# Kernel optimization log

Measured on AMD Instinct MI355X. Metric: run time of the kernel, lower is better.

Reference implementation:

```python
import jax, jax.numpy as jnp
import numpy as np

TOP_K = 8
N_EXPERTS = 64
ALPHA = 0.001
EPS = 1e-9


def setup_inputs() -> dict:
    key = jax.random.key(0)
    k1, k2 = jax.random.split(key)
    B, S, H, E = 4, 4096, 2048, N_EXPERTS
    hidden_states = jax.random.normal(k1, (B, S, H), dtype=jnp.float32)
    # kaiming_uniform_(a=sqrt(5)) on [E,H] -> bound = 1/sqrt(H)
    bound = 1.0 / np.sqrt(H)
    weight = jax.random.uniform(k2, (E, H), dtype=jnp.float32, minval=-bound, maxval=bound)
    return {"hidden_states": hidden_states, "weight": weight}


def reference(hidden_states, weight):
    B, S, H = hidden_states.shape
    E = weight.shape[0]
    x = hidden_states.reshape(-1, H)                     # [N, H], N = B*S
    logits = jnp.einsum('nh,eh->ne', x, weight)          # [N, E]
    scores = jax.nn.sigmoid(logits)                      # sigmoid affinity (DeepSeek-V3 style)

    topk_weight, topk_idx = jax.lax.top_k(scores, TOP_K)  # [N, K]
    # norm_topk_prob = True and top_k > 1
    denom = topk_weight.sum(axis=-1, keepdims=True) + EPS
    topk_weight = topk_weight / denom

    # aux load-balance loss (training, alpha > 0); scatter-count instead of one_hot
    N = x.shape[0]
    counts = jnp.zeros((E,), dtype=jnp.float32).at[topk_idx.reshape(-1)].add(1.0)
    load = counts / (N * TOP_K)                          # == one_hot.mean(dim=(0,1))
    prob_raw = scores / (scores.sum(axis=-1, keepdims=True) + EPS)
    prob = prob_raw.mean(axis=0)
    prob = prob / (prob.sum() + EPS)
    aux_loss = ALPHA * (load * prob).sum() * E

    return topk_idx, topk_weight, aux_loss
```

## Files before the change

kernel.cpp:

```cpp
#include <hip/hip_runtime.h>
#include <math.h>

#define N_TOK 16384
#define HDIM  2048
#define NEXP  64
#define TOPK  8
#define NKS   4
#define KSEG  (HDIM / NKS)

#define PART_OFF  0
#define WT_OFF    (32u << 20)
#define STATS_OFF (33u << 20)

typedef double d4 __attribute__((ext_vector_type(4)));

__global__ __launch_bounds__(256) void conv_wt_kernel(const float* __restrict__ W,
                                                      double* __restrict__ Wt) {
    int i = blockIdx.x * 256 + threadIdx.x;
    int k = i >> 6, e = i & 63;
    Wt[i] = (double)W[(size_t)e * HDIM + k];
}

__global__ void mfma_probe_kernel(int* __restrict__ flag) {
    const int l = threadIdx.x;
    const int i16 = l & 15, q = l >> 4;
    const int r4 = l >> 2,  m4 = l & 3;
    int fv = 0;
#pragma unroll
    for (int ai = 0; ai < 2; ++ai)
#pragma unroll
    for (int bi = 0; bi < 2; ++bi) {
        const int ra = ai ? r4 : i16, ka = ai ? m4 : q;
        const int cb = bi ? r4 : i16, kb = bi ? m4 : q;
        double a = (double)(ra * 4 + ka + 1);
        double b = (double)((kb + 1) * 100 + 3 * cb);
        d4 acc = {0., 0., 0., 0.};
        acc = __builtin_amdgcn_mfma_f64_16x16x4f64(a, b, acc, 0, 0, 0);
#pragma unroll
        for (int sf = 0; sf < 2; ++sf)
#pragma unroll
        for (int tr = 0; tr < 2; ++tr) {
            int ok = 1;
#pragma unroll
            for (int r = 0; r < 4; ++r) {
                const int p   = sf ? (q + 4 * r) : (4 * q + r);
                const int row = tr ? i16 : p;
                const int col = tr ? p : i16;
                double ref = 0.0;
#pragma unroll
                for (int k = 0; k < 4; ++k)
                    ref += (double)(row * 4 + k + 1) * (double)((k + 1) * 100 + 3 * col);
                ok &= (acc[r] == ref);
            }
            if (__all(ok) && fv == 0) fv = 1 + ai * 8 + bi * 4 + sf * 2 + tr;
        }
    }
    if (l == 0) *flag = fv;
}

__global__ __launch_bounds__(256) void gemm_mfma_kernel(const float* __restrict__ X,
                                                        const double* __restrict__ Wt,
                                                        const int* __restrict__ flag,
                                                        double* __restrict__ part) {
    const int f = *flag;
    if (f == 0) return;
    const int fb = f - 1;
    const int ai = (fb >> 3) & 1, bi = (fb >> 2) & 1;
    const int sf = (fb >> 1) & 1, tr = fb & 1;

    const int tt  = blockIdx.x >> 2;
    const int ks  = blockIdx.x & 3;
    const int tid = threadIdx.x;
    const int l   = tid & 63;
    const int wv  = tid >> 6;
    const int wr  = wv >> 1, wc = wv & 1;
    const int tok0 = tt * 64;
    const int k0   = ks * KSEG;

    const int i16 = l & 15, q = l >> 4, r4 = l >> 2, m4 = l & 3;
    const int ra = ai ? r4 : i16, ka = ai ? m4 : q;
    const int cb = bi ? r4 : i16, kb = bi ? m4 : q;

    __shared__ double xs[64][34];
    __shared__ double wsh[32][66];

    d4 acc[2][2];
#pragma unroll
    for (int i = 0; i < 2; ++i)
#pragma unroll
        for (int j = 0; j < 2; ++j) acc[i][j] = (d4){0., 0., 0., 0.};

    const int xr = tid >> 2;
    const int xc = (tid & 3) * 8;
    const float* xg = X + (size_t)(tok0 + xr) * HDIM + k0 + xc;
    const int wk = tid >> 3;
    const int we = (tid & 7) * 8;
    const double* wg = Wt + (size_t)(k0 + wk) * NEXP + we;

    float4  px0 = *(const float4*)xg;
    float4  px1 = *(const float4*)(xg + 4);
    double2 pw0 = *(const double2*)(wg);
    double2 pw1 = *(const double2*)(wg + 2);
    double2 pw2 = *(const double2*)(wg + 4);
    double2 pw3 = *(const double2*)(wg + 6);

    const double* pa0 = &xs[wr * 32 + ra][ka];
    const double* pa1 = &xs[wr * 32 + 16 + ra][ka];
    const double* pb0 = &wsh[kb][wc * 32 + cb];
    const double* pb1 = &wsh[kb][wc * 32 + 16 + cb];

    for (int c = 0; c < KSEG / 32; ++c) {
        __syncthreads();
        {
            double2 t;
            t.x = (double)px0.x; t.y = (double)px0.y; *(double2*)&xs[xr][xc]     = t;
            t.x = (double)px0.z; t.y = (double)px0.w; *(double2*)&xs[xr][xc + 2] = t;
            t.x = (double)px1.x; t.y = (double)px1.y; *(double2*)&xs[xr][xc + 4] = t;
            t.x = (double)px1.z; t.y = (double)px1.w; *(double2*)&xs[xr][xc + 6] = t;
            *(double2*)&wsh[wk][we]     = pw0;
            *(double2*)&wsh[wk][we + 2] = pw1;
            *(double2*)&wsh[wk][we + 4] = pw2;
            *(double2*)&wsh[wk][we + 6] = pw3;
        }
        __syncthreads();
        if (c + 1 < KSEG / 32) {
            const float*  xn = xg + (c + 1) * 32;
            const double* wn = wg + (size_t)(c + 1) * 32 * NEXP;
            px0 = *(const float4*)xn;
            px1 = *(const float4*)(xn + 4);
            pw0 = *(const double2*)(wn);
            pw1 = *(const double2*)(wn + 2);
            pw2 = *(const double2*)(wn + 4);
            pw3 = *(const double2*)(wn + 6);
        }
#pragma unroll
        for (int kq = 0; kq < 8; ++kq) {
            double a0 = pa0[kq * 4];
            double a1 = pa1[kq * 4];
            double b0 = pb0[(size_t)kq * 4 * 66];
            double b1 = pb1[(size_t)kq * 4 * 66];
            acc[0][0] = __builtin_amdgcn_mfma_f64_16x16x4f64(a0, b0, acc[0][0], 0, 0, 0);
            acc[0][1] = __builtin_amdgcn_mfma_f64_16x16x4f64(a0, b1, acc[0][1], 0, 0, 0);
            acc[1][0] = __builtin_amdgcn_mfma_f64_16x16x4f64(a1, b0, acc[1][0], 0, 0, 0);
            acc[1][1] = __builtin_amdgcn_mfma_f64_16x16x4f64(a1, b1, acc[1][1], 0, 0, 0);
        }
    }

    double* pbase = part + (size_t)ks * N_TOK * NEXP;
#pragma unroll
    for (int rt = 0; rt < 2; ++rt)
#pragma unroll
        for (int ct = 0; ct < 2; ++ct)
#pragma unroll
            for (int r = 0; r < 4; ++r) {
                const int p    = sf ? (q + 4 * r) : (4 * q + r);
                const int dtok = tr ? i16 : p;
                const int dex  = tr ? p : i16;
                const int tok  = tok0 + wr * 32 + rt * 16 + dtok;
                const int ex   = wc * 32 + ct * 16 + dex;
                pbase[(size_t)tok * NEXP + ex] = acc[rt][ct][r];
            }
}

__global__ __launch_bounds__(512, 4) void gemm_valu_kernel(const float* __restrict__ X,
                                                           const double* __restrict__ Wt,
                                                           const int* __restrict__ flag,
                                                           double* __restrict__ part) {
    if (*flag != 0) return;
    const int tt   = blockIdx.x >> 2;
    const int ks   = blockIdx.x & 3;
    const int tid  = threadIdx.x;
    const int lane = tid & 63;
    const int wv   = tid >> 6;
    const int tok0 = tt * 64;
    const int k0   = ks * KSEG;

    __shared__ double xs[64][18];
    __shared__ double wsh[16][66];

    double acc[8];
#pragma unroll
    for (int t = 0; t < 8; ++t) acc[t] = 0.0;

    const int sx_tok = tid >> 3;
    const int sx_k   = (tid & 7) * 2;
    const float* xg  = X + (size_t)(tok0 + sx_tok) * HDIM + k0 + sx_k;
    const int sw_k = tid >> 5;
    const int sw_e = (tid & 31) * 2;
    const double* wg = Wt + (size_t)(k0 + sw_k) * NEXP + sw_e;

    float2  px = *(const float2*)xg;
    double2 pw = *(const double2*)wg;

    for (int c = 0; c < KSEG / 16; ++c) {
        __syncthreads();
        {
            double2 xv; xv.x = (double)px.x; xv.y = (double)px.y;
            *(double2*)&xs[sx_tok][sx_k] = xv;
            *(double2*)&wsh[sw_k][sw_e]  = pw;
        }
        __syncthreads();
        if (c + 1 < KSEG / 16) {
            px = *(const float2*)(xg + (c + 1) * 16);
            pw = *(const double2*)(wg + (size_t)(c + 1) * 16 * NEXP);
        }
        double wr_[16];
#pragma unroll
        for (int j = 0; j < 16; ++j) wr_[j] = wsh[j][lane];
#pragma unroll
        for (int t = 0; t < 8; ++t) {
            const int tr = wv * 8 + t;
#pragma unroll
            for (int kp = 0; kp < 8; ++kp) {
                double2 xv = *(const double2*)&xs[tr][kp * 2];
                acc[t] = fma(xv.x, wr_[kp * 2],     acc[t]);
                acc[t] = fma(xv.y, wr_[kp * 2 + 1], acc[t]);
            }
        }
    }

    double* pb = part + ((size_t)ks * N_TOK + tok0 + wv * 8) * NEXP + lane;
#pragma unroll
    for (int t = 0; t < 8; ++t)
        pb[(size_t)t * NEXP] = acc[t];
}

__global__ __launch_bounds__(256) void topk_kernel(const double* __restrict__ part,
                                                   float* __restrict__ outIdx,
                                                   float* __restrict__ outW,
                                                   float* __restrict__ stats) {
    __shared__ float sc_s[32][65];
    __shared__ float lds_counts[NEXP];
    __shared__ float psum_part[4][NEXP];
    const int tid  = threadIdx.x;
    const int lane = tid & 63;
    const int w    = tid >> 6;
    if (tid < NEXP) lds_counts[tid] = 0.f;

    const int t0 = blockIdx.x * 32;
#pragma unroll
    for (int p = 0; p < 8; ++p) {
        const int idx = p * 256 + tid;
        const int t   = idx >> 6;
        const int e   = idx & 63;
        const double* pp = part + ((size_t)(t0 + t)) * NEXP + e;
        double l = (pp[0] + pp[(size_t)N_TOK * NEXP]) +
                   (pp[2 * (size_t)N_TOK * NEXP] + pp[3 * (size_t)N_TOK * NEXP]);
        sc_s[t][e] = (float)(1.0 / (1.0 + exp(-l)));
    }
    __syncthreads();

    float ps = 0.f;
    for (int i = 0; i < 8; ++i) {
        const int tloc = w * 8 + i;
        const int t    = t0 + tloc;
        float s = sc_s[tloc][lane];

        float rs = s;
#pragma unroll
        for (int off = 32; off; off >>= 1) rs += __shfl_xor(rs, off);
        ps += s / (rs + 1e-9f);

        float cur = s;
        float denom = 0.f;
        int   wi = 0;
        float wv = 0.f;
#pragma unroll
        for (int k = 0; k < TOPK; ++k) {
            float m = cur; int mi = lane;
#pragma unroll
            for (int off = 32; off; off >>= 1) {
                float om = __shfl_xor(m, off);
                int   oi = __shfl_xor(mi, off);
                if (om > m || (om == m && oi < mi)) { m = om; mi = oi; }
            }
            denom += m;
            if (lane == k)  { wi = mi; wv = m; }
            if (lane == mi) cur = -1e30f;
        }
        if (lane < TOPK) {
            outIdx[(size_t)t * TOPK + lane] = (float)wi;
            outW  [(size_t)t * TOPK + lane] = wv / (denom + 1e-9f);
            atomicAdd(&lds_counts[wi], 1.f);
        }
    }
    psum_part[w][lane] = ps;
    __syncthreads();
    if (tid < NEXP) {
        float tot = psum_part[0][tid] + psum_part[1][tid] +
                    psum_part[2][tid] + psum_part[3][tid];
        atomicAdd(&stats[tid], tot);
        atomicAdd(&stats[NEXP + tid], lds_counts[tid]);
    }
}

__global__ void aux_kernel(const float* __restrict__ stats, float* __restrict__ out) {
    const int e = threadIdx.x;
    float prob = stats[e] / (float)N_TOK;
    float cnt  = stats[NEXP + e];
    float loadf = cnt / ((float)N_TOK * TOPK);
    float S = prob;
#pragma unroll
    for (int off = 32; off; off >>= 1) S += __shfl_xor(S, off);
    float pn = prob / (S + 1e-9f);
    float v  = loadf * pn;
#pragma unroll
    for (int off = 32; off; off >>= 1) v += __shfl_xor(v, off);
    if (e == 0) out[2 * N_TOK * TOPK] = 0.001f * v * (float)NEXP;
}

extern "C" void kernel_launch(void* const* d_in, const int* in_sizes, int n_in,
                              void* d_out, int out_size, void* d_ws, size_t ws_size,
                              hipStream_t stream) {
    (void)in_sizes; (void)n_in; (void)out_size; (void)ws_size;
    const float* X = (const float*)d_in[0];
    const float* W = (const float*)d_in[1];
    float* out = (float*)d_out;
    char*  ws  = (char*)d_ws;
    double* part  = (double*)(ws + PART_OFF);
    double* Wt    = (double*)(ws + WT_OFF);
    float*  stats = (float*)(ws + STATS_OFF);
    int*    flag  = (int*)(stats + 128);

    hipMemsetAsync(stats, 0, 132 * sizeof(float), stream);
    conv_wt_kernel<<<512, 256, 0, stream>>>(W, Wt);
    mfma_probe_kernel<<<1, 64, 0, stream>>>(flag);
    gemm_mfma_kernel<<<1024, 256, 0, stream>>>(X, Wt, flag, part);
    gemm_valu_kernel<<<1024, 512, 0, stream>>>(X, Wt, flag, part);
    topk_kernel<<<512, 256, 0, stream>>>(part, out, out + N_TOK * TOPK, stats);
    aux_kernel<<<1, 64, 0, stream>>>(stats, out);
}
```

Measured before the change: 148.5 us.

## Drop weight transpose kernel; read fp32 weights directly with k-permuted shared layout

Removes the separate kernel that converted the weight matrix to a transposed fp64 copy. Both GEMM kernels now load the fp32 weights directly from their original [E,H] layout and convert to double while staging into shared memory. The MFMA kernel stores X and W tiles with the same k-major-per-row layout, using a permuted k ordering so each lane can fetch two operands per double2 LDS read. This saves one kernel launch and a workspace round trip, but the global weight loads become scalar strided reads.

New measurement: 154.0 us. 3.7% more time.

```diff
diff --git a/kernel.cpp b/kernel.cpp
--- a/kernel.cpp
+++ b/kernel.cpp
@@ -7,19 +7,13 @@
 #define TOPK  8
 #define NKS   4
 #define KSEG  (HDIM / NKS)
+#define KCH   32
+#define NCH   (KSEG / KCH)
 
 #define PART_OFF  0
-#define WT_OFF    (32u << 20)
 #define STATS_OFF (33u << 20)
 
 typedef double d4 __attribute__((ext_vector_type(4)));
-
-__global__ __launch_bounds__(256) void conv_wt_kernel(const float* __restrict__ W,
-                                                      double* __restrict__ Wt) {
-    int i = blockIdx.x * 256 + threadIdx.x;
-    int k = i >> 6, e = i & 63;
-    Wt[i] = (double)W[(size_t)e * HDIM + k];
-}
 
 __global__ void mfma_probe_kernel(int* __restrict__ flag) {
     const int l = threadIdx.x;
@@ -59,7 +53,7 @@
 }
 
 __global__ __launch_bounds__(256) void gemm_mfma_kernel(const float* __restrict__ X,
-                                                        const double* __restrict__ Wt,
+                                                        const float* __restrict__ W,
                                                         const int* __restrict__ flag,
                                                         double* __restrict__ part) {
     const int f = *flag;
@@ -81,8 +75,8 @@
     const int ra = ai ? r4 : i16, ka = ai ? m4 : q;
     const int cb = bi ? r4 : i16, kb = bi ? m4 : q;
 
-    __shared__ double xs[64][34];
-    __shared__ double wsh[32][66];
+    __shared__ double Xs[64][34];
+    __shared__ double Ws[64][34];
 
     d4 acc[2][2];
 #pragma unroll
@@ -90,59 +84,58 @@
 #pragma unroll
         for (int j = 0; j < 2; ++j) acc[i][j] = (d4){0., 0., 0., 0.};
 
-    const int xr = tid >> 2;
-    const int xc = (tid & 3) * 8;
-    const float* xg = X + (size_t)(tok0 + xr) * HDIM + k0 + xc;
-    const int wk = tid >> 3;
-    const int we = (tid & 7) * 8;
-    const double* wg = Wt + (size_t)(k0 + wk) * NEXP + we;
-
-    float4  px0 = *(const float4*)xg;
-    float4  px1 = *(const float4*)(xg + 4);
-    double2 pw0 = *(const double2*)(wg);
-    double2 pw1 = *(const double2*)(wg + 2);
-    double2 pw2 = *(const double2*)(wg + 4);
-    double2 pw3 = *(const double2*)(wg + 6);
-
-    const double* pa0 = &xs[wr * 32 + ra][ka];
-    const double* pa1 = &xs[wr * 32 + 16 + ra][ka];
-    const double* pb0 = &wsh[kb][wc * 32 + cb];
-    const double* pb1 = &wsh[kb][wc * 32 + 16 + cb];
-
-    for (int c = 0; c < KSEG / 32; ++c) {
+    const int rs = tid >> 2, cu = tid & 3;
+    const float* xg = X + (size_t)(tok0 + rs) * HDIM + k0 + cu;
+    const float* wg = W + (size_t)rs * HDIM + k0 + cu;
+
+    float fx[8], fw[8];
+#pragma unroll
+    for (int j = 0; j < 4; ++j) {
+        fx[2 * j]     = xg[8 * j];
+        fx[2 * j + 1] = xg[8 * j + 4];
+        fw[2 * j]     = wg[8 * j];
+        fw[2 * j + 1] = wg[8 * j + 4];
+    }
+
+    for (int c = 0; c < NCH; ++c) {
         __syncthreads();
-        {
-            double2 t;
-            t.x = (double)px0.x; t.y = (double)px0.y; *(double2*)&xs[xr][xc]     = t;
-            t.x = (double)px0.z; t.y = (double)px0.w; *(double2*)&xs[xr][xc + 2] = t;
-            t.x = (double)px1.x; t.y = (double)px1.y; *(double2*)&xs[xr][xc + 4] = t;
-            t.x = (double)px1.z; t.y = (double)px1.w; *(double2*)&xs[xr][xc + 6] = t;
-            *(double2*)&wsh[wk][we]     = pw0;
-            *(double2*)&wsh[wk][we + 2] = pw1;
-            *(double2*)&wsh[wk][we + 4] = pw2;
-            *(double2*)&wsh[wk][we + 6] = pw3;
+#pragma unroll
+        for (int j = 0; j < 4; ++j) {
+            double2 dx; dx.x = (double)fx[2 * j]; dx.y = (double)fx[2 * j + 1];
+            double2 dw; dw.x = (double)fw[2 * j]; dw.y = (double)fw[2 * j + 1];
+            *(double2*)&Xs[rs][8 * cu + 2 * j] = dx;
+            *(double2*)&Ws[rs][8 * cu + 2 * j] = dw;
         }
         __syncthreads();
-        if (c + 1 < KSEG / 32) {
-            const float*  xn = xg + (c + 1) * 32;
-            const double* wn = wg + (size_t)(c + 1) * 32 * NEXP;
-            px0 = *(const float4*)xn;
-            px1 = *(const float4*)(xn + 4);
-            pw0 = *(const double2*)(wn);
-            pw1 = *(const double2*)(wn + 2);
-            pw2 = *(const double2*)(wn + 4);
-            pw3 = *(const double2*)(wn + 6);
-        }
-#pragma unroll
-        for (int kq = 0; kq < 8; ++kq) {
-            double a0 = pa0[kq * 4];
-            double a1 = pa1[kq * 4];
-            double b0 = pb0[(size_t)kq * 4 * 66];
-            double b1 = pb1[(size_t)kq * 4 * 66];
-            acc[0][0] = __builtin_amdgcn_mfma_f64_16x16x4f64(a0, b0, acc[0][0], 0, 0, 0);
-            acc[0][1] = __builtin_amdgcn_mfma_f64_16x16x4f64(a0, b1, acc[0][1], 0, 0, 0);
-            acc[1][0] = __builtin_amdgcn_mfma_f64_16x16x4f64(a1, b0, acc[1][0], 0, 0, 0);
-            acc[1][1] = __builtin_amdgcn_mfma_f64_16x16x4f64(a1, b1, acc[1][1], 0, 0, 0);
+        if (c + 1 < NCH) {
+            const float* xn = xg + (c + 1) * KCH;
+            const float* wn = wg + (c + 1) * KCH;
+#pragma unroll
+            for (int j = 0; j < 4; ++j) {
+                fx[2 * j]     = xn[8 * j];
+                fx[2 * j + 1] = xn[8 * j + 4];
+                fw[2 * j]     = wn[8 * j];
+                fw[2 * j + 1] = wn[8 * j + 4];
+            }
+        }
+        const double* pa0 = &Xs[wr * 32 + ra][8 * ka];
+        const double* pa1 = &Xs[wr * 32 + 16 + ra][8 * ka];
+        const double* pb0 = &Ws[wc * 32 + cb][8 * kb];
+        const double* pb1 = &Ws[wc * 32 + 16 + cb][8 * kb];
+#pragma unroll
+        for (int t = 0; t < 4; ++t) {
+            double2 a0 = *(const double2*)(pa0 + 2 * t);
+            double2 a1 = *(const double2*)(pa1 + 2 * t);
+            double2 b0 = *(const double2*)(pb0 + 2 * t);
+            double2 b1 = *(const double2*)(pb1 + 2 * t);
+            acc[0][0] = __builtin_amdgcn_mfma_f64_16x16x4f64(a0.x, b0.x, acc[0][0], 0, 0, 0);
+            acc[0][1] = __builtin_amdgcn_mfma_f64_16x16x4f64(a0.x, b1.x, acc[0][1], 0, 0, 0);
+            acc[1][0] = __builtin_amdgcn_mfma_f64_16x16x4f64(a1.x, b0.x, acc[1][0], 0, 0, 0);
+            acc[1][1] = __builtin_amdgcn_mfma_f64_16x16x4f64(a1.x, b1.x, acc[1][1], 0, 0, 0);
+            acc[0][0] = __builtin_amdgcn_mfma_f64_16x16x4f64(a0.y, b0.y, acc[0][0], 0, 0, 0);
+            acc[0][1] = __builtin_amdgcn_mfma_f64_16x16x4f64(a0.y, b1.y, acc[0][1], 0, 0, 0);
+            acc[1][0] = __builtin_amdgcn_mfma_f64_16x16x4f64(a1.y, b0.y, acc[1][0], 0, 0, 0);
+            acc[1][1] = __builtin_amdgcn_mfma_f64_16x16x4f64(a1.y, b1.y, acc[1][1], 0, 0, 0);
         }
     }
 
@@ -163,7 +156,7 @@
 }
 
 __global__ __launch_bounds__(512, 4) void gemm_valu_kernel(const float* __restrict__ X,
-                                                           const double* __restrict__ Wt,
+                                                           const float* __restrict__ W,
                                                            const int* __restrict__ flag,
                                                            double* __restrict__ part) {
     if (*flag != 0) return;
@@ -187,32 +180,35 @@
     const float* xg  = X + (size_t)(tok0 + sx_tok) * HDIM + k0 + sx_k;
     const int sw_k = tid >> 5;
     const int sw_e = (tid & 31) * 2;
-    const double* wg = Wt + (size_t)(k0 + sw_k) * NEXP + sw_e;
-
-    float2  px = *(const float2*)xg;
-    double2 pw = *(const double2*)wg;
+    const float* wg0 = W + (size_t)sw_e * HDIM + k0 + sw_k;
+    const float* wg1 = W + (size_t)(sw_e + 1) * HDIM + k0 + sw_k;
+
+    float2 px = *(const float2*)xg;
+    float  pa = *wg0, pb2 = *wg1;
 
     for (int c = 0; c < KSEG / 16; ++c) {
         __syncthreads();
         {
             double2 xv; xv.x = (double)px.x; xv.y = (double)px.y;
             *(double2*)&xs[sx_tok][sx_k] = xv;
-            *(double2*)&wsh[sw_k][sw_e]  = pw;
+            double2 wv2; wv2.x = (double)pa; wv2.y = (double)pb2;
+            *(double2*)&wsh[sw_k][sw_e] = wv2;
         }
         __syncthreads();
         if (c + 1 < KSEG / 16) {
-            px = *(const float2*)(xg + (c + 1) * 16);
-            pw = *(const double2*)(wg + (size_t)(c + 1) * 16 * NEXP);
+            px  = *(const float2*)(xg + (c + 1) * 16);
+            pa  = wg0[(c + 1) * 16];
+            pb2 = wg1[(c + 1) * 16];
         }
         double wr_[16];
 #pragma unroll
         for (int j = 0; j < 16; ++j) wr_[j] = wsh[j][lane];
 #pragma unroll
         for (int t = 0; t < 8; ++t) {
-            const int tr = wv * 8 + t;
+            const int trr = wv * 8 + t;
 #pragma unroll
             for (int kp = 0; kp < 8; ++kp) {
-                double2 xv = *(const double2*)&xs[tr][kp * 2];
+                double2 xv = *(const double2*)&xs[trr][kp * 2];
                 acc[t] = fma(xv.x, wr_[kp * 2],     acc[t]);
                 acc[t] = fma(xv.y, wr_[kp * 2 + 1], acc[t]);
             }
@@ -264,7 +260,7 @@
         float cur = s;
         float denom = 0.f;
         int   wi = 0;
-        float wv = 0.f;
+        float wvv = 0.f;
 #pragma unroll
         for (int k = 0; k < TOPK; ++k) {
             float m = cur; int mi = lane;
@@ -275,12 +271,12 @@
                 if (om > m || (om == m && oi < mi)) { m = om; mi = oi; }
             }
             denom += m;
-            if (lane == k)  { wi = mi; wv = m; }
+            if (lane == k)  { wi = mi; wvv = m; }
             if (lane == mi) cur = -1e30f;
         }
         if (lane < TOPK) {
             outIdx[(size_t)t * TOPK + lane] = (float)wi;
-            outW  [(size_t)t * TOPK + lane] = wv / (denom + 1e-9f);
+            outW  [(size_t)t * TOPK + lane] = wvv / (denom + 1e-9f);
             atomicAdd(&lds_counts[wi], 1.f);
         }
     }
@@ -318,15 +314,13 @@
     float* out = (float*)d_out;
     char*  ws  = (char*)d_ws;
     double* part  = (double*)(ws + PART_OFF);
-    double* Wt    = (double*)(ws + WT_OFF);
     float*  stats = (float*)(ws + STATS_OFF);
     int*    flag  = (int*)(stats + 128);
 
     hipMemsetAsync(stats, 0, 132 * sizeof(float), stream);
-    conv_wt_kernel<<<512, 256, 0, stream>>>(W, Wt);
     mfma_probe_kernel<<<1, 64, 0, stream>>>(flag);
-    gemm_mfma_kernel<<<1024, 256, 0, stream>>>(X, Wt, flag, part);
-    gemm_valu_kernel<<<1024, 512, 0, stream>>>(X, Wt, flag, part);
+    gemm_mfma_kernel<<<1024, 256, 0, stream>>>(X, W, flag, part);
+    gemm_valu_kernel<<<1024, 512, 0, stream>>>(X, W, flag, part);
     topk_kernel<<<512, 256, 0, stream>>>(part, out, out + N_TOK * TOPK, stats);
     aux_kernel<<<1, 64, 0, stream>>>(stats, out);
 }
```
